# Kernel tuning notes

Measured on AMD Instinct MI355X. Metric: run time of the kernel, lower is better.

Reference implementation:

```python
import jax, jax.numpy as jnp
import numpy as np

B, S, H, NH = 8, 512, 4096, 64
HD = H // NH  # head dim = 64
LN_EPS = 1e-12
TOL_BITS = 16


def quant16(x):
    """Per-tensor dynamic fixed-point quantization to 16 bits.

    int_bit_width = ceil(log2(max|x|)) + 1 (sign bit); frac = 16 - int_bits.
    Values are rounded to the fixed-point grid and clipped to int16 range.
    """
    m = jnp.max(jnp.abs(x))
    int_bw = jnp.ceil(jnp.log2(jnp.maximum(m, 1e-12))) + 1.0
    frac_bw = jnp.asarray(TOL_BITS, x.dtype) - int_bw
    scale = jnp.exp2(frac_bw).astype(x.dtype)
    q = jnp.clip(jnp.round(x * scale), -32768.0, 32767.0) / scale
    return q


def setup_inputs() -> dict:
    key = jax.random.key(0)
    ks = jax.random.split(key, 6)
    s = 0.02
    return {
        "input_ids": jax.random.normal(ks[0], (B, S, H), jnp.float32),
        "attention_mask": jnp.zeros((B, 1, 1, S), jnp.float32),
        "Wq": jax.random.normal(ks[1], (H, H), jnp.float32) * s,
        "bq": jnp.zeros((H,), jnp.float32),
        "Wk": jax.random.normal(ks[2], (H, H), jnp.float32) * s,
        "bk": jnp.zeros((H,), jnp.float32),
        "Wv": jax.random.normal(ks[3], (H, H), jnp.float32) * s,
        "bv": jnp.zeros((H,), jnp.float32),
        "Wd": jax.random.normal(ks[4], (H, H), jnp.float32) * s,
        "bd": jnp.zeros((H,), jnp.float32),
        "ln_w": jnp.ones((H,), jnp.float32),
        "ln_b": jnp.zeros((H,), jnp.float32),
    }


def reference(input_ids, attention_mask, Wq, bq, Wk, bk, Wv, bv, Wd, bd, ln_w, ln_b):
    x = input_ids  # [B,S,H]
    # Q/K/V projections (torch Linear: y = x @ W.T + b), each followed by quant
    q = quant16(jnp.einsum('bsh,oh->bso', x, Wq) + bq)
    k = quant16(jnp.einsum('bsh,oh->bso', x, Wk) + bk)
    v = quant16(jnp.einsum('bsh,oh->bso', x, Wv) + bv)
    # split heads -> [B,NH,S,HD]
    q = q.reshape(B, S, NH, HD).transpose(0, 2, 1, 3)
    k = k.reshape(B, S, NH, HD).transpose(0, 2, 1, 3)
    v = v.reshape(B, S, NH, HD).transpose(0, 2, 1, 3)
    scores = jnp.einsum('bnqd,bnkd->bnqk', q, k) / np.sqrt(HD).astype(np.float32)
    scores = quant16(scores)
    scores = scores + attention_mask
    probs = jax.nn.softmax(scores, axis=-1)
    probs = quant16(probs)
    ctx = quant16(jnp.einsum('bnqk,bnkd->bnqd', probs, v))
    ctx = ctx.transpose(0, 2, 1, 3)  # [B,S,NH,HD]
    # dense: w = Wd.T reshaped to (NH, HD, H)
    w = Wd.T.reshape(NH, HD, H)
    proj = quant16(jnp.einsum('bfnd,ndh->bfh', ctx, w) + bd)
    # residual + LayerNorm
    y = x + proj
    mu = jnp.mean(y, axis=-1, keepdims=True)
    var = jnp.mean(jnp.square(y - mu), axis=-1, keepdims=True)
    y = (y - mu) / jnp.sqrt(var + LN_EPS) * ln_w + ln_b
    return quant16(y)
```

## Files before the change

### kernel.cpp

```cpp
#include <hip/hip_runtime.h>
#include <hip/hip_bf16.h>
#include <stdint.h>


typedef __attribute__((ext_vector_type(4))) float f32x4;
typedef __attribute__((ext_vector_type(8))) __bf16 bf16x8;

__device__ inline unsigned short f2bf(float f) {
  union { float f; unsigned u; } c; c.f = f;
  unsigned r = (c.u + 0x7fffu + ((c.u >> 16) & 1u)) >> 16;
  return (unsigned short)r;
}

__device__ inline float bf2f(unsigned short s) {
  union { unsigned u; float f; } c; c.u = ((unsigned)s) << 16;
  return c.f;
}

__device__ inline void gload_lds16(const void* g, void* l) {
  __builtin_amdgcn_global_load_lds(
      (const __attribute__((address_space(1))) void*)g,
      (__attribute__((address_space(3))) void*)l, 16, 0, 0);
}

__global__ __launch_bounds__(256) void conv_all(
    const float* __restrict__ x, const float* __restrict__ wq,
    const float* __restrict__ wk, const float* __restrict__ wv,
    const float* __restrict__ wd, unsigned short* __restrict__ out) {
  int i = blockIdx.x * 256 + threadIdx.x;
  int reg = i >> 21;
  int off = i & 2097151;
  const float* src = (reg == 0) ? x : (reg == 1) ? wq : (reg == 2) ? wk
                     : (reg == 3) ? wv : wd;
  const float4* ip = (const float4*)src;
  float4 a = ip[off * 2], b = ip[off * 2 + 1];
  union { unsigned short s[8]; uint4 v; } o;
  o.s[0] = f2bf(a.x); o.s[1] = f2bf(a.y); o.s[2] = f2bf(a.z); o.s[3] = f2bf(a.w);
  o.s[4] = f2bf(b.x); o.s[5] = f2bf(b.y); o.s[6] = f2bf(b.z); o.s[7] = f2bf(b.w);
  ((uint4*)out)[i] = o.v;
}

template <int BIAS_MODE>
__global__ __launch_bounds__(512, 2) void gemm_4p(
    const unsigned short* __restrict__ A, const unsigned short* __restrict__ Bw,
    const float* __restrict__ bias0, const float* __restrict__ bias1,
    const float* __restrict__ bias2, unsigned short* __restrict__ Cout,
    int M, int N, int K) {
  extern __shared__ unsigned short lds[];
  const int nbm = M >> 8, nbn = N >> 8, nwg = nbm * nbn;
  const int bid = blockIdx.x;
  const int wg = (bid & 7) * (nwg >> 3) + (bid >> 3);
  const int bm = wg % nbm, bn = wg / nbm;
  const int tid = threadIdx.x, w = tid >> 6, l = tid & 63;
  const int wr = w >> 2, wc = w & 3;
  const int lr = l & 15, lg = l >> 4;
  const unsigned short* gA = A + (size_t)bm * 256 * K;
  const unsigned short* gB = Bw + (size_t)bn * 256 * K;
  const int NT = K >> 6;
  const int srow = tid >> 3;
  const int scol = ((tid & 7) ^ (srow & 7)) << 3;
  f32x4 acc[8][4] = {};
  bf16x8 a[8], b[8];

#define STG(op, buf, h, kt)                                                    \
  {                                                                            \
    const unsigned short* g_ = (op) ? gB : gA;                                 \
    _Pragma("unroll")                                                          \
    for (int j_ = 0; j_ < 2; ++j_) {                                           \
      gload_lds16(                                                             \
          g_ + (size_t)((h) * 128 + j_ * 64 + srow) * K + (kt) * 64 + scol,    \
          &lds[((op) * 2 + (buf)) * 16384 + ((h) * 128 + j_ * 64) * 64 +       \
               w * 512]);                                                      \
    }                                                                          \
  }

#define RDA(buf, m, kk)                                                        \
  (*(const bf16x8*)&lds[(buf) * 16384 + (wr * 128 + (m) * 16 + lr) * 64 +      \
                        ((((kk) * 4 + lg) ^ (lr & 7)) << 3)])
#define RDB(buf, n, kk)                                                        \
  (*(const bf16x8*)&lds[(2 + (buf)) * 16384 + (wc * 64 + (n) * 16 + lr) * 64 + \
                        ((((kk) * 4 + lg) ^ (lr & 7)) << 3)])

#define LDA(buf, mh)                                                           \
  _Pragma("unroll")                                                            \
  for (int m_ = 0; m_ < 4; ++m_) {                                             \
    a[m_ * 2 + 0] = RDA(buf, (mh) * 4 + m_, 0);                                \
    a[m_ * 2 + 1] = RDA(buf, (mh) * 4 + m_, 1);                                \
  }
#define LDB(buf, nh)                                                           \
  _Pragma("unroll")                                                            \
  for (int n_ = 0; n_ < 2; ++n_) {                                             \
    b[((nh) * 2 + n_) * 2 + 0] = RDB(buf, (nh) * 2 + n_, 0);                   \
    b[((nh) * 2 + n_) * 2 + 1] = RDB(buf, (nh) * 2 + n_, 1);                   \
  }

#define MM(mbase, nbase)                                                       \
  __builtin_amdgcn_s_setprio(1);                                               \
  _Pragma("unroll")                                                            \
  for (int m_ = 0; m_ < 4; ++m_) {                                             \
    _Pragma("unroll")                                                          \
    for (int n_ = 0; n_ < 2; ++n_) {                                           \
      acc[(mbase) + m_][(nbase) + n_] =                                        \
          __builtin_amdgcn_mfma_f32_16x16x32_bf16(                             \
              a[m_ * 2], b[((nbase) + n_) * 2], acc[(mbase) + m_][(nbase) + n_],\
              0, 0, 0);                                                        \
      acc[(mbase) + m_][(nbase) + n_] =                                        \
          __builtin_amdgcn_mfma_f32_16x16x32_bf16(                             \
              a[m_ * 2 + 1], b[((nbase) + n_) * 2 + 1],                        \
              acc[(mbase) + m_][(nbase) + n_], 0, 0, 0);                       \
    }                                                                          \
  }                                                                            \
  __builtin_amdgcn_s_setprio(0);

#define BAR() __builtin_amdgcn_s_barrier()
#define VMW4() asm volatile("s_waitcnt vmcnt(4)" ::: "memory")
#define VMW0() asm volatile("s_waitcnt vmcnt(0)" ::: "memory")

  STG(0, 0, 0, 0); STG(0, 0, 1, 0); STG(1, 0, 0, 0); STG(1, 0, 1, 0);
  STG(1, 1, 0, 1); STG(1, 1, 1, 1);
  VMW4();
  BAR();

  const int NI = NT >> 1;
  for (int i = 0; i < NI; ++i) {
    const int t1 = 2 * i + 1, t2 = 2 * i + 2, t3 = 2 * i + 3;
    const bool s2 = t2 < NT, s3 = t3 < NT;
    LDA(0, 0); LDB(0, 0); LDB(0, 1);
    STG(0, 1, 0, t1); STG(0, 1, 1, t1);
    BAR();
    MM(0, 0); MM(0, 2);
    LDA(0, 1);
    if (s2) { STG(1, 0, 0, t2); STG(1, 0, 1, t2); VMW4(); } else VMW0();
    BAR();
    MM(4, 0); MM(4, 2);
    LDA(1, 0); LDB(1, 0); LDB(1, 1);
    if (s2) { STG(0, 0, 0, t2); STG(0, 0, 1, t2); }
    BAR();
    MM(0, 0); MM(0, 2);
    LDA(1, 1);
    if (s3) { STG(1, 1, 0, t3); STG(1, 1, 1, t3); VMW4(); }
    else if (s2) VMW0();
    BAR();
    MM(4, 0); MM(4, 2);
  }

  __syncthreads();
  unsigned short* Cb = lds + w * 8192;
#pragma unroll
  for (int n = 0; n < 4; ++n) {
    int col = bn * 256 + wc * 64 + n * 16 + lr;
    float bv = 0.f;
    if (BIAS_MODE == 1) bv = bias0[col];
    else if (BIAS_MODE == 2)
      bv = (col < 4096) ? bias0[col] : (col < 8192 ? bias1[col - 4096] : bias2[col - 8192]);
#pragma unroll
    for (int m = 0; m < 8; ++m)
#pragma unroll
      for (int r = 0; r < 4; ++r) {
        int row = m * 16 + lg * 4 + r;
        int c2 = n * 16 + lr;
        Cb[row * 64 + (c2 ^ ((row & 7) << 3))] = f2bf(acc[m][n][r] + bv);
      }
  }
#pragma unroll
  for (int j = 0; j < 16; ++j) {
    int i16 = j * 64 + l;
    int row = i16 >> 3;
    int g = i16 & 7;
    uint4 v = *(const uint4*)&Cb[row * 64 + ((g * 8) ^ ((row & 7) << 3))];
    int grow = bm * 256 + wr * 128 + row;
    int gcol = bn * 256 + wc * 64 + g * 8;
    *(uint4*)&Cout[(size_t)grow * N + gcol] = v;
  }
#undef STG
#undef RDA
#undef RDB
#undef LDA
#undef LDB
#undef MM
#undef BAR
#undef VMW4
#undef VMW0
}

__global__ __launch_bounds__(512) void attn_kernel(
    const unsigned short* __restrict__ qkv, const float* __restrict__ mask,
    unsigned short* __restrict__ ctx) {
  extern __shared__ char smem[];
  unsigned short* Kt = (unsigned short*)smem;
  unsigned short* Vt = Kt + 512 * 64;
  unsigned short* Pb = Vt + 64 * 512;
  float* Mb = (float*)(Pb + 8 * 16 * 64);

  const int bid = blockIdx.x;
  const int b = bid >> 6, h = bid & 63;
  const int tid = threadIdx.x, w = tid >> 6, l = tid & 63;
  const size_t tokbase = (size_t)b * 512;

  Mb[tid < 512 ? tid : 0] = mask[b * 512 + (tid < 512 ? tid : 0)];
#pragma unroll
  for (int it = 0; it < 8; ++it) {
    int idx = it * 512 + tid;
    int row = idx >> 3, g = (idx & 7) << 3;
    const unsigned short* src = qkv + (tokbase + row) * 12288 + 4096 + h * 64 + g;
    uint4 v = *(const uint4*)src;
    *(uint4*)&Kt[row * 64 + (g ^ ((row & 7) << 3))] = v;
  }
#pragma unroll
  for (int it = 0; it < 8; ++it) {
    int idx = it * 512 + tid;
    int key = idx >> 3, g = (idx & 7) << 3;
    const unsigned short* src = qkv + (tokbase + key) * 12288 + 8192 + h * 64 + g;
    uint4 v = *(const uint4*)src;
    const unsigned short* e = (const unsigned short*)&v;
#pragma unroll
    for (int i = 0; i < 8; i++) {
      int d = g + i;
      Vt[d * 512 + (key ^ ((d & 7) << 3))] = e[i];
    }
  }
  __syncthreads();

  unsigned short* Pw = Pb + w * 16 * 64;
  const int lr = l & 15, lg = l >> 4;

  for (int c = 0; c < 4; ++c) {
    int q0 = w * 64 + c * 16;
    const unsigned short* qsrc = qkv + (tokbase + q0 + lr) * 12288 + h * 64 + lg * 8;
    bf16x8 qa0 = *(const bf16x8*)qsrc;
    bf16x8 qa1 = *(const bf16x8*)(qsrc + 32);
    f32x4 sc[32];
    f32x4 zero = {0.f, 0.f, 0.f, 0.f};
    __builtin_amdgcn_s_setprio(1);
#pragma unroll
    for (int n = 0; n < 32; n++) {
      int key = n * 16 + lr;
      bf16x8 kb0 = *(const bf16x8*)&Kt[key * 64 + ((lg * 8) ^ ((key & 7) << 3))];
      bf16x8 kb1 = *(const bf16x8*)&Kt[key * 64 + ((32 + lg * 8) ^ ((key & 7) << 3))];
      f32x4 a = __builtin_amdgcn_mfma_f32_16x16x32_bf16(qa0, kb0, zero, 0, 0, 0);
      sc[n] = __builtin_amdgcn_mfma_f32_16x16x32_bf16(qa1, kb1, a, 0, 0, 0);
    }
    __builtin_amdgcn_s_setprio(0);
    float rmax[4] = {-1e30f, -1e30f, -1e30f, -1e30f};
#pragma unroll
    for (int n = 0; n < 32; n++) {
      float mk = Mb[n * 16 + lr];
#pragma unroll
      for (int r = 0; r < 4; r++) {
        float s = sc[n][r] * 0.125f + mk;
        sc[n][r] = s;
        rmax[r] = fmaxf(rmax[r], s);
      }
    }
#pragma unroll
    for (int r = 0; r < 4; r++) {
      float m = rmax[r];
      m = fmaxf(m, __shfl_xor(m, 8)); m = fmaxf(m, __shfl_xor(m, 4));
      m = fmaxf(m, __shfl_xor(m, 2)); m = fmaxf(m, __shfl_xor(m, 1));
      rmax[r] = m;
    }
    float rsum[4] = {0.f, 0.f, 0.f, 0.f};
#pragma unroll
    for (int n = 0; n < 32; n++)
#pragma unroll
      for (int r = 0; r < 4; r++) {
        float p = __expf(sc[n][r] - rmax[r]);
        sc[n][r] = p;
        rsum[r] += p;
      }
#pragma unroll
    for (int r = 0; r < 4; r++) {
      float s = rsum[r];
      s += __shfl_xor(s, 8); s += __shfl_xor(s, 4);
      s += __shfl_xor(s, 2); s += __shfl_xor(s, 1);
      rsum[r] = s;
    }
    f32x4 cacc[4] = {};
#pragma unroll
    for (int kb = 0; kb < 8; ++kb) {
#pragma unroll
      for (int nn = 0; nn < 4; ++nn) {
        int colp = nn * 16 + lr;
#pragma unroll
        for (int r = 0; r < 4; r++) {
          int m = lg * 4 + r;
          Pw[m * 64 + (colp ^ ((m & 7) << 3))] = f2bf(sc[kb * 4 + nn][r]);
        }
      }
      bf16x8 pa0 = *(const bf16x8*)&Pw[lr * 64 + ((lg * 8) ^ ((lr & 7) << 3))];
      bf16x8 pa1 = *(const bf16x8*)&Pw[lr * 64 + ((32 + lg * 8) ^ ((lr & 7) << 3))];
      __builtin_amdgcn_s_setprio(1);
#pragma unroll
      for (int dt = 0; dt < 4; ++dt) {
        int vr = dt * 16 + lr;
        int k0 = kb * 64 + lg * 8;
        bf16x8 vb0 = *(const bf16x8*)&Vt[vr * 512 + (k0 ^ ((vr & 7) << 3))];
        bf16x8 vb1 = *(const bf16x8*)&Vt[vr * 512 + ((k0 + 32) ^ ((vr & 7) << 3))];
        cacc[dt] = __builtin_amdgcn_mfma_f32_16x16x32_bf16(pa0, vb0, cacc[dt], 0, 0, 0);
        cacc[dt] = __builtin_amdgcn_mfma_f32_16x16x32_bf16(pa1, vb1, cacc[dt], 0, 0, 0);
      }
      __builtin_amdgcn_s_setprio(0);
    }
#pragma unroll
    for (int dt = 0; dt < 4; ++dt)
#pragma unroll
      for (int r = 0; r < 4; r++) {
        int m = lg * 4 + r;
        int c2 = dt * 16 + lr;
        Pw[m * 64 + (c2 ^ ((m & 7) << 3))] = f2bf(cacc[dt][r] / rsum[r]);
      }
#pragma unroll
    for (int j = 0; j < 2; ++j) {
      int i16 = j * 64 + l;
      int row = i16 >> 3;
      int g = i16 & 7;
      uint4 v = *(const uint4*)&Pw[row * 64 + ((g * 8) ^ ((row & 7) << 3))];
      *(uint4*)&ctx[(tokbase + q0 + row) * 4096 + h * 64 + g * 8] = v;
    }
  }
}

__global__ __launch_bounds__(256) void ln_kernel(
    const unsigned short* __restrict__ xb, const unsigned short* __restrict__ proj,
    float* __restrict__ out,
    const float* __restrict__ lnw, const float* __restrict__ lnb) {
  int t = blockIdx.x;
  const uint4* xr = (const uint4*)(xb + (size_t)t * 4096);
  const uint4* pr = (const uint4*)(proj + (size_t)t * 4096);
  float y[16];
  float sum = 0.f, sq = 0.f;
#pragma unroll
  for (int j = 0; j < 2; j++) {
    int i8 = j * 256 + threadIdx.x;
    uint4 xv = xr[i8];
    uint4 pv = pr[i8];
    const unsigned short* xs = (const unsigned short*)&xv;
    const unsigned short* ps = (const unsigned short*)&pv;
#pragma unroll
    for (int e = 0; e < 8; ++e) {
      float yy = bf2f(xs[e]) + bf2f(ps[e]);
      y[j * 8 + e] = yy;
      sum += yy;
      sq += yy * yy;
    }
  }
#pragma unroll
  for (int off = 32; off >= 1; off >>= 1) {
    sum += __shfl_down(sum, off);
    sq += __shfl_down(sq, off);
  }
  __shared__ float red[8];
  int w = threadIdx.x >> 6, l = threadIdx.x & 63;
  if (l == 0) { red[w] = sum; red[4 + w] = sq; }
  __syncthreads();
  float ts = red[0] + red[1] + red[2] + red[3];
  float tq = red[4] + red[5] + red[6] + red[7];
  float mean = ts * (1.f / 4096.f);
  float var = tq * (1.f / 4096.f) - mean * mean;
  float rs = rsqrtf(var + 1e-12f);
  float4* orow = (float4*)(out + (size_t)t * 4096);
#pragma unroll
  for (int j = 0; j < 2; j++) {
    int i8 = j * 256 + threadIdx.x;
#pragma unroll
    for (int hh = 0; hh < 2; ++hh) {
      int i4 = i8 * 2 + hh;
      float4 wv = ((const float4*)lnw)[i4];
      float4 bb = ((const float4*)lnb)[i4];
      float4 o;
      o.x = (y[j * 8 + hh * 4 + 0] - mean) * rs * wv.x + bb.x;
      o.y = (y[j * 8 + hh * 4 + 1] - mean) * rs * wv.y + bb.y;
      o.z = (y[j * 8 + hh * 4 + 2] - mean) * rs * wv.z + bb.z;
      o.w = (y[j * 8 + hh * 4 + 3] - mean) * rs * wv.w + bb.w;
      orow[i4] = o;
    }
  }
}

extern "C" void kernel_launch(void* const* d_in, const int* in_sizes, int n_in,
                              void* d_out, int out_size, void* d_ws, size_t ws_size,
                              hipStream_t stream) {
  const float* x   = (const float*)d_in[0];
  const float* msk = (const float*)d_in[1];
  const float* Wq  = (const float*)d_in[2];
  const float* bq  = (const float*)d_in[3];
  const float* Wk  = (const float*)d_in[4];
  const float* bk  = (const float*)d_in[5];
  const float* Wv  = (const float*)d_in[6];
  const float* bv  = (const float*)d_in[7];
  const float* Wd  = (const float*)d_in[8];
  const float* bd  = (const float*)d_in[9];
  const float* lnw = (const float*)d_in[10];
  const float* lnb = (const float*)d_in[11];
  float* out = (float*)d_out;

  unsigned short* xb    = (unsigned short*)d_ws;
  unsigned short* wqkvb = xb + (size_t)16777216;
  unsigned short* wdb   = wqkvb + (size_t)50331648;
  unsigned short* qkvb  = wdb + (size_t)16777216;
  unsigned short* ctxb  = wqkvb;
  unsigned short* projb = qkvb;

  conv_all<<<40960, 256, 0, stream>>>(x, Wq, Wk, Wv, Wd, xb);

  (void)hipFuncSetAttribute((const void*)(gemm_4p<2>),
                            hipFuncAttributeMaxDynamicSharedMemorySize, 131072);
  (void)hipFuncSetAttribute((const void*)(gemm_4p<1>),
                            hipFuncAttributeMaxDynamicSharedMemorySize, 131072);

  gemm_4p<2><<<768, 512, 131072, stream>>>(xb, wqkvb, bq, bk, bv, qkvb,
                                           4096, 12288, 4096);

  (void)hipFuncSetAttribute((const void*)attn_kernel,
                            hipFuncAttributeMaxDynamicSharedMemorySize, 149504);
  attn_kernel<<<512, 512, 149504, stream>>>(qkvb, msk, ctxb);

  gemm_4p<1><<<256, 512, 131072, stream>>>(ctxb, wdb, bd, nullptr, nullptr,
                                           projb, 4096, 4096, 4096);

  ln_kernel<<<4096, 256, 0, stream>>>(xb, projb, out, lnw, lnb);
}
```

Measured before the change: 639.5 us.

## Triple-buffer the A operand in the GEMM LDS pipeline for deeper prefetch

The GEMM now keeps the A tile in a three-slot LDS ring while B stays double-buffered, and stages whole 256-row tiles per load macro. A tiles are fetched two K-steps ahead, where the old version loaded the next A tile just before use, so global-load latency has more room to hide behind the MFMA work. Dynamic LDS per block grows from 128KB to 160KB. That uses the full per-CU LDS budget and rules out two resident blocks, while the ring indexing and vmcnt waits are retuned to match.

```diff
diff --git a/kernel.cpp b/kernel.cpp
--- a/kernel.cpp
+++ b/kernel.cpp
@@ -41,7 +41,7 @@
 }
 
 template <int BIAS_MODE>
-__global__ __launch_bounds__(512, 2) void gemm_4p(
+__global__ __launch_bounds__(512, 2) void gemm_a3(
     const unsigned short* __restrict__ A, const unsigned short* __restrict__ Bw,
     const float* __restrict__ bias0, const float* __restrict__ bias1,
     const float* __restrict__ bias2, unsigned short* __restrict__ Cout,
@@ -62,30 +62,36 @@
   f32x4 acc[8][4] = {};
   bf16x8 a[8], b[8];
 
-#define STG(op, buf, h, kt)                                                    \
+#define STGA(ring, kt)                                                         \
   {                                                                            \
-    const unsigned short* g_ = (op) ? gB : gA;                                 \
     _Pragma("unroll")                                                          \
-    for (int j_ = 0; j_ < 2; ++j_) {                                           \
-      gload_lds16(                                                             \
-          g_ + (size_t)((h) * 128 + j_ * 64 + srow) * K + (kt) * 64 + scol,    \
-          &lds[((op) * 2 + (buf)) * 16384 + ((h) * 128 + j_ * 64) * 64 +       \
-               w * 512]);                                                      \
+    for (int h_ = 0; h_ < 4; ++h_) {                                           \
+      gload_lds16(gA + (size_t)(h_ * 64 + srow) * K + (kt) * 64 + scol,        \
+                  &lds[(ring) * 16384 + (h_ * 64) * 64 + w * 512]);            \
     }                                                                          \
   }
-
-#define RDA(buf, m, kk)                                                        \
-  (*(const bf16x8*)&lds[(buf) * 16384 + (wr * 128 + (m) * 16 + lr) * 64 +      \
+#define STGB(buf, kt)                                                          \
+  {                                                                            \
+    _Pragma("unroll")                                                          \
+    for (int h_ = 0; h_ < 4; ++h_) {                                           \
+      gload_lds16(gB + (size_t)(h_ * 64 + srow) * K + (kt) * 64 + scol,        \
+                  &lds[49152 + (buf) * 16384 + (h_ * 64) * 64 + w * 512]);     \
+    }                                                                          \
+  }
+
+#define RDA(ring, m, kk)                                                       \
+  (*(const bf16x8*)&lds[(ring) * 16384 + (wr * 128 + (m) * 16 + lr) * 64 +     \
                         ((((kk) * 4 + lg) ^ (lr & 7)) << 3)])
 #define RDB(buf, n, kk)                                                        \
-  (*(const bf16x8*)&lds[(2 + (buf)) * 16384 + (wc * 64 + (n) * 16 + lr) * 64 + \
+  (*(const bf16x8*)&lds[49152 + (buf) * 16384 +                                \
+                        (wc * 64 + (n) * 16 + lr) * 64 +                       \
                         ((((kk) * 4 + lg) ^ (lr & 7)) << 3)])
 
-#define LDA(buf, mh)                                                           \
+#define LDA(ring, mh)                                                          \
   _Pragma("unroll")                                                            \
   for (int m_ = 0; m_ < 4; ++m_) {                                             \
-    a[m_ * 2 + 0] = RDA(buf, (mh) * 4 + m_, 0);                                \
-    a[m_ * 2 + 1] = RDA(buf, (mh) * 4 + m_, 1);                                \
+    a[m_ * 2 + 0] = RDA(ring, (mh) * 4 + m_, 0);                               \
+    a[m_ * 2 + 1] = RDA(ring, (mh) * 4 + m_, 1);                               \
   }
 #define LDB(buf, nh)                                                           \
   _Pragma("unroll")                                                            \
@@ -113,35 +119,38 @@
   __builtin_amdgcn_s_setprio(0);
 
 #define BAR() __builtin_amdgcn_s_barrier()
-#define VMW4() asm volatile("s_waitcnt vmcnt(4)" ::: "memory")
+#define VMW8() asm volatile("s_waitcnt vmcnt(8)" ::: "memory")
 #define VMW0() asm volatile("s_waitcnt vmcnt(0)" ::: "memory")
 
-  STG(0, 0, 0, 0); STG(0, 0, 1, 0); STG(1, 0, 0, 0); STG(1, 0, 1, 0);
-  STG(1, 1, 0, 1); STG(1, 1, 1, 1);
-  VMW4();
+  STGA(0, 0); STGB(0, 0); STGA(1, 1); STGB(1, 1);
+  VMW8();
   BAR();
 
   const int NI = NT >> 1;
+  int r0 = 0;
   for (int i = 0; i < NI; ++i) {
-    const int t1 = 2 * i + 1, t2 = 2 * i + 2, t3 = 2 * i + 3;
+    const int t2 = 2 * i + 2, t3 = 2 * i + 3;
     const bool s2 = t2 < NT, s3 = t3 < NT;
-    LDA(0, 0); LDB(0, 0); LDB(0, 1);
-    STG(0, 1, 0, t1); STG(0, 1, 1, t1);
+    const int r1 = (r0 + 1 == 3) ? 0 : r0 + 1;
+    const int r2 = (r1 + 1 == 3) ? 0 : r1 + 1;
+    LDA(r0, 0); LDB(0, 0); LDB(0, 1);
+    if (s2) STGA(r2, t2);
     BAR();
     MM(0, 0); MM(0, 2);
-    LDA(0, 1);
-    if (s2) { STG(1, 0, 0, t2); STG(1, 0, 1, t2); VMW4(); } else VMW0();
+    LDA(r0, 1);
+    if (s2) { STGB(0, t2); VMW8(); } else VMW0();
     BAR();
     MM(4, 0); MM(4, 2);
-    LDA(1, 0); LDB(1, 0); LDB(1, 1);
-    if (s2) { STG(0, 0, 0, t2); STG(0, 0, 1, t2); }
+    LDA(r1, 0); LDB(1, 0); LDB(1, 1);
+    if (s3) STGA(r0, t3);
     BAR();
     MM(0, 0); MM(0, 2);
-    LDA(1, 1);
-    if (s3) { STG(1, 1, 0, t3); STG(1, 1, 1, t3); VMW4(); }
+    LDA(r1, 1);
+    if (s3) { STGB(1, t3); VMW8(); }
     else if (s2) VMW0();
     BAR();
     MM(4, 0); MM(4, 2);
+    r0 = r2;
   }
 
   __syncthreads();
@@ -172,14 +181,15 @@
     int gcol = bn * 256 + wc * 64 + g * 8;
     *(uint4*)&Cout[(size_t)grow * N + gcol] = v;
   }
-#undef STG
+#undef STGA
+#undef STGB
 #undef RDA
 #undef RDB
 #undef LDA
 #undef LDB
 #undef MM
 #undef BAR
-#undef VMW4
+#undef VMW8
 #undef VMW0
 }
 
@@ -403,19 +413,19 @@
 
   conv_all<<<40960, 256, 0, stream>>>(x, Wq, Wk, Wv, Wd, xb);
 
-  (void)hipFuncSetAttribute((const void*)(gemm_4p<2>),
-                            hipFuncAttributeMaxDynamicSharedMemorySize, 131072);
-  (void)hipFuncSetAttribute((const void*)(gemm_4p<1>),
-                            hipFuncAttributeMaxDynamicSharedMemorySize, 131072);
-
-  gemm_4p<2><<<768, 512, 131072, stream>>>(xb, wqkvb, bq, bk, bv, qkvb,
+  (void)hipFuncSetAttribute((const void*)(gemm_a3<2>),
+                            hipFuncAttributeMaxDynamicSharedMemorySize, 163840);
+  (void)hipFuncSetAttribute((const void*)(gemm_a3<1>),
+                            hipFuncAttributeMaxDynamicSharedMemorySize, 163840);
+
+  gemm_a3<2><<<768, 512, 163840, stream>>>(xb, wqkvb, bq, bk, bv, qkvb,
                                            4096, 12288, 4096);
 
   (void)hipFuncSetAttribute((const void*)attn_kernel,
                             hipFuncAttributeMaxDynamicSharedMemorySize, 149504);
   attn_kernel<<<512, 512, 149504, stream>>>(qkvb, msk, ctxb);
 
-  gemm_4p<1><<<256, 512, 131072, stream>>>(ctxb, wdb, bd, nullptr, nullptr,
+  gemm_a3<1><<<256, 512, 163840, stream>>>(ctxb, wdb, bd, nullptr, nullptr,
                                            projb, 4096, 4096, 4096);
 
   ln_kernel<<<4096, 256, 0, stream>>>(xb, projb, out, lnw, lnb);
```

Result: no change. 650.1 us (+1.7%).
